# Performance work log

Measured on AMD Instinct MI355X. Metric: run time of the kernel, lower is better.

## Reference

```python
import jax, jax.numpy as jnp
import numpy as np


def setup_inputs() -> dict:
    key = jax.random.key(0)
    k1, k2 = jax.random.split(key)
    x = jax.random.normal(k1, (8, 64, 256, 256), dtype=jnp.float32)
    grid = jax.random.normal(k2, (8, 256, 256, 2), dtype=jnp.float32)
    return {"x": x, "grid": grid}


def _warp_bilinear_zeros(x, grid):
    # x: [N, C, H, W]; grid: [N, Ho, Wo, 2] with (dx, dy) pixel offsets.
    N, C, H, W = x.shape
    Ho, Wo = grid.shape[1], grid.shape[2]
    dt = grid.dtype
    base_y = jnp.arange(Ho, dtype=dt)[:, None]   # [Ho, 1]
    base_x = jnp.arange(Wo, dtype=dt)[None, :]   # [1, Wo]
    abs_x = grid[..., 0] + base_x                # [N, Ho, Wo]
    abs_y = grid[..., 1] + base_y
    # normalize then unnormalize (align_corners=True), matching the torch chain
    norm_x = abs_x * 2 / (W - 1) - 1
    norm_y = abs_y * 2 / (H - 1) - 1
    ix = (norm_x + 1) * 0.5 * (W - 1)
    iy = (norm_y + 1) * 0.5 * (H - 1)

    x0 = jnp.floor(ix); x1 = x0 + 1
    y0 = jnp.floor(iy); y1 = y0 + 1
    wx1 = ix - x0; wx0 = 1 - wx1
    wy1 = iy - y0; wy0 = 1 - wy1

    inb_x0 = (x0 >= 0) & (x0 <= W - 1)
    inb_x1 = (x1 >= 0) & (x1 <= W - 1)
    inb_y0 = (y0 >= 0) & (y0 <= H - 1)
    inb_y1 = (y1 >= 0) & (y1 <= H - 1)

    xi0 = jnp.clip(x0, 0, W - 1).astype(jnp.int32)
    xi1 = jnp.clip(x1, 0, W - 1).astype(jnp.int32)
    yi0 = jnp.clip(y0, 0, H - 1).astype(jnp.int32)
    yi1 = jnp.clip(y1, 0, H - 1).astype(jnp.int32)

    def gather(img, yi, xi):  # img [C,H,W], yi/xi [Ho,Wo] -> [C,Ho,Wo]
        return img[:, yi, xi]
    g = jax.vmap(gather)

    # zeros padding: mask out-of-bounds corner contributions
    w00 = (wy0 * wx0 * (inb_y0 & inb_x0).astype(dt))[:, None]  # [N,1,Ho,Wo]
    w01 = (wy0 * wx1 * (inb_y0 & inb_x1).astype(dt))[:, None]
    w10 = (wy1 * wx0 * (inb_y1 & inb_x0).astype(dt))[:, None]
    w11 = (wy1 * wx1 * (inb_y1 & inb_x1).astype(dt))[:, None]

    out = (g(x, yi0, xi0) * w00 + g(x, yi0, xi1) * w01
           + g(x, yi1, xi0) * w10 + g(x, yi1, xi1) * w11)
    return out  # [N, C, Ho, Wo]


def reference(x, grid):
    return _warp_bilinear_zeros(x, grid)
```

## Files before the change

kernel.cpp:

```cpp
#include <hip/hip_runtime.h>


#define N_ 8
#define C_ 64
#define H_ 256
#define W_ 256
#define HO_ 256
#define WO_ 256

__global__ __launch_bounds__(256) void gridsample_kernel(
    const float* __restrict__ x,
    const float2* __restrict__ grid2,
    float* __restrict__ out)
{
    const int sp = blockIdx.x * blockDim.x + threadIdx.x;
    const int total = N_ * HO_ * WO_;
    if (sp >= total) return;

    const int wo = sp % WO_;
    const int t  = sp / WO_;
    const int ho = t % HO_;
    const int n  = t / HO_;

    const float2 g = grid2[sp];
    const float dx = g.x;
    const float dy = g.y;

    const float absx = dx + (float)wo;
    const float absy = dy + (float)ho;
    const float normx = absx * 2.0f / (float)(W_ - 1) - 1.0f;
    const float normy = absy * 2.0f / (float)(H_ - 1) - 1.0f;
    const float ix = (normx + 1.0f) * 0.5f * (float)(W_ - 1);
    const float iy = (normy + 1.0f) * 0.5f * (float)(H_ - 1);

    const float x0f = floorf(ix);
    const float y0f = floorf(iy);
    const float x1f = x0f + 1.0f;
    const float y1f = y0f + 1.0f;

    const float wx1 = ix - x0f, wx0 = 1.0f - wx1;
    const float wy1 = iy - y0f, wy0 = 1.0f - wy1;

    const bool inx0 = (x0f >= 0.0f) && (x0f <= (float)(W_ - 1));
    const bool inx1 = (x1f >= 0.0f) && (x1f <= (float)(W_ - 1));
    const bool iny0 = (y0f >= 0.0f) && (y0f <= (float)(H_ - 1));
    const bool iny1 = (y1f >= 0.0f) && (y1f <= (float)(H_ - 1));

    const int xi0 = min(max((int)x0f, 0), W_ - 1);
    const int xi1 = min(max((int)x1f, 0), W_ - 1);
    const int yi0 = min(max((int)y0f, 0), H_ - 1);
    const int yi1 = min(max((int)y1f, 0), H_ - 1);

    const float w00 = wy0 * wx0 * ((iny0 && inx0) ? 1.0f : 0.0f);
    const float w01 = wy0 * wx1 * ((iny0 && inx1) ? 1.0f : 0.0f);
    const float w10 = wy1 * wx0 * ((iny1 && inx0) ? 1.0f : 0.0f);
    const float w11 = wy1 * wx1 * ((iny1 && inx1) ? 1.0f : 0.0f);

    const int o00 = yi0 * W_ + xi0;
    const int o01 = yi0 * W_ + xi1;
    const int o10 = yi1 * W_ + xi0;
    const int o11 = yi1 * W_ + xi1;

    const float* __restrict__ xb = x + (size_t)n * C_ * H_ * W_;
    float* __restrict__ ob = out + (size_t)n * C_ * HO_ * WO_ + (size_t)ho * WO_ + wo;

    #pragma unroll 4
    for (int c = 0; c < C_; ++c) {
        const float* __restrict__ xc = xb + (size_t)c * H_ * W_;
        const float v = xc[o00] * w00 + xc[o01] * w01
                      + xc[o10] * w10 + xc[o11] * w11;
        ob[(size_t)c * HO_ * WO_] = v;
    }
}

extern "C" void kernel_launch(void* const* d_in, const int* in_sizes, int n_in,
                              void* d_out, int out_size, void* d_ws, size_t ws_size,
                              hipStream_t stream) {
    const float*  x    = (const float*)d_in[0];
    const float2* grid = (const float2*)d_in[1];
    float*        out  = (float*)d_out;

    const int total = N_ * HO_ * WO_;
    const int block = 256;
    const int nblocks = (total + block - 1) / block;
    gridsample_kernel<<<nblocks, block, 0, stream>>>(x, grid, out);
}
```

Baseline: 310.0 us.

## Split channels into chunks of 8 and map blocks to XCDs for L2 locality

Each block now handles one output row for an 8-channel chunk of one image, so the grid grows eightfold, each thread does less serial gather work, and the machine gets more parallelism. The block index is swizzled so that consecutive blocks on the same XCD (b&7) cover the same (n, channel-chunk) planes, keeping each XCD's gathers inside a small input working set for L2 reuse. The cost is that the grid coordinates and bilinear weights are recomputed once per channel chunk.

Result: faster. 294.1 us (-5.1%).

```diff
diff --git a/kernel.cpp b/kernel.cpp
--- a/kernel.cpp
+++ b/kernel.cpp
@@ -7,21 +7,24 @@
 #define W_ 256
 #define HO_ 256
 #define WO_ 256
+#define CCH 8
+#define NCC (C_ / CCH)
 
 __global__ __launch_bounds__(256) void gridsample_kernel(
     const float* __restrict__ x,
     const float2* __restrict__ grid2,
     float* __restrict__ out)
 {
-    const int sp = blockIdx.x * blockDim.x + threadIdx.x;
-    const int total = N_ * HO_ * WO_;
-    if (sp >= total) return;
+    const int b    = blockIdx.x;
+    const int xcd  = b & 7;
+    const int idx  = b >> 3;
+    const int plane = xcd * (NCC * N_ / 8) + (idx >> 8);
+    const int ho   = idx & 255;
+    const int n    = plane >> 3;
+    const int cc   = plane & 7;
+    const int wo   = threadIdx.x;
 
-    const int wo = sp % WO_;
-    const int t  = sp / WO_;
-    const int ho = t % HO_;
-    const int n  = t / HO_;
-
+    const int sp = (n * HO_ + ho) * WO_ + wo;
     const float2 g = grid2[sp];
     const float dx = g.x;
     const float dy = g.y;
@@ -61,15 +64,18 @@
     const int o10 = yi1 * W_ + xi0;
     const int o11 = yi1 * W_ + xi1;
 
-    const float* __restrict__ xb = x + (size_t)n * C_ * H_ * W_;
-    float* __restrict__ ob = out + (size_t)n * C_ * HO_ * WO_ + (size_t)ho * WO_ + wo;
+    const int c0 = cc * CCH;
+    const float* __restrict__ xb =
+        x + ((size_t)n * C_ + c0) * (H_ * W_);
+    float* __restrict__ ob =
+        out + (((size_t)n * C_ + c0) * HO_ + ho) * WO_ + wo;
 
-    #pragma unroll 4
-    for (int c = 0; c < C_; ++c) {
-        const float* __restrict__ xc = xb + (size_t)c * H_ * W_;
+    #pragma unroll
+    for (int c = 0; c < CCH; ++c) {
+        const float* __restrict__ xc = xb + (size_t)c * (H_ * W_);
         const float v = xc[o00] * w00 + xc[o01] * w01
                       + xc[o10] * w10 + xc[o11] * w11;
-        ob[(size_t)c * HO_ * WO_] = v;
+        ob[(size_t)c * (HO_ * WO_)] = v;
     }
 }
 
@@ -80,8 +86,6 @@
     const float2* grid = (const float2*)d_in[1];
     float*        out  = (float*)d_out;
 
-    const int total = N_ * HO_ * WO_;
-    const int block = 256;
-    const int nblocks = (total + block - 1) / block;
-    gridsample_kernel<<<nblocks, block, 0, stream>>>(x, grid, out);
+    const int nblocks = N_ * NCC * HO_;
+    gridsample_kernel<<<nblocks, 256, 0, stream>>>(x, grid, out);
 }
```
